# Optimization experiments

Measured on AMD Instinct MI355X. Metric: run time of the kernel, lower is better.

## Reference

```python
import jax, jax.numpy as jnp
import numpy as np

DIM = 1024
FF = 4096
BATCH = 4
SEQ = 2048
EPS = 1e-5


def setup_inputs() -> dict:
    key = jax.random.key(0)
    ks = jax.random.split(key, 8)
    x = jax.random.normal(ks[0], (BATCH, SEQ, DIM), dtype=jnp.float32)
    # phazor init: exp(2j*pi*arange(dim)/dim) * |randn(dim)|
    ang = 2.0 * np.pi * jnp.arange(DIM, dtype=jnp.float32) / DIM
    mag = jnp.abs(jax.random.normal(ks[1], (DIM,), dtype=jnp.float32))
    phazor_re = mag * jnp.cos(ang)
    phazor_im = mag * jnp.sin(ang)
    last_re = jax.random.normal(ks[2], (DIM,), dtype=jnp.float32)
    last_im = jax.random.normal(ks[3], (DIM,), dtype=jnp.float32)
    w1 = jax.random.normal(ks[4], (FF, DIM), dtype=jnp.float32) * DIM ** -0.5
    b1 = jnp.zeros((FF,), dtype=jnp.float32)
    w2 = jax.random.normal(ks[5], (DIM, FF), dtype=jnp.float32) * FF ** -0.5
    b2 = jnp.zeros((DIM,), dtype=jnp.float32)
    return {
        'x': x,
        'ln1_w': jnp.ones((DIM,), jnp.float32), 'ln1_b': jnp.zeros((DIM,), jnp.float32),
        'ln2_w': jnp.ones((DIM,), jnp.float32), 'ln2_b': jnp.zeros((DIM,), jnp.float32),
        'sc_lin': jnp.ones((DIM,), jnp.float32),
        'phazor_re': phazor_re, 'phazor_im': phazor_im,
        'last_re': last_re, 'last_im': last_im,
        'w1': w1, 'b1': b1, 'w2': w2, 'b2': b2,
    }


def _layer_norm(x, w, b):
    mu = jnp.mean(x, axis=-1, keepdims=True)
    var = jnp.mean(jnp.square(x - mu), axis=-1, keepdims=True)
    return (x - mu) * jax.lax.rsqrt(var + EPS) * w + b


def _sconv(x, phazor_re, phazor_im, last_re, last_im):
    B, L, D = x.shape
    dtype = x.dtype
    xc = x.astype(jnp.complex64)
    p_raw = phazor_re + 1j * phazor_im
    # tanh(|p|) * exp(i*angle(p))
    p = (jnp.tanh(jnp.abs(p_raw)) * jnp.exp(1j * jnp.angle(p_raw))).astype(jnp.complex64)
    t = jnp.arange(L)[:, None]
    prog = jnp.power(p[None, :], t)            # [L, D] complex
    filt_fft = jnp.fft.fft(prog, n=2 * L, axis=0)   # [2L, D]
    x_fft = jnp.fft.fft(xc, n=2 * L, axis=1)        # [B, 2L, D]
    conv = jnp.fft.ifft(filt_fft[None] * x_fft, axis=1)[:, :L]  # [B, L, D]
    last = (last_re + 1j * last_im)[None, None, :]  # [1,1,D] broadcast over batch
    conv_with_past = conv + last * prog[None] * p[None, None]
    return conv_with_past.real.astype(dtype)


def reference(x, ln1_w, ln1_b, ln2_w, ln2_b, sc_lin,
              phazor_re, phazor_im, last_re, last_im,
              w1, b1, w2, b2):
    # SConv branch
    x_res = x
    h = _layer_norm(x, ln1_w, ln1_b)
    h = jax.nn.silu(h)
    h = _sconv(h, phazor_re, phazor_im, last_re, last_im)
    h = h * sc_lin
    x = h + x_res
    # FFN branch
    x_res = x
    h = _layer_norm(x, ln2_w, ln2_b)
    h = jax.nn.silu(jnp.einsum('bld,fd->blf', h, w1) + b1)
    h = jnp.einsum('blf,df->bld', h, w2) + b2
    return h + x_res
```

## Files before the change

### kernel.cpp

```cpp
#include <hip/hip_runtime.h>
#include <cmath>


#define DIMD 1024
#define FFD  4096
#define BATCH 4
#define SEQL 2048
#define MROWS (BATCH*SEQL)
#define EPSF 1e-5f
#define CHUNKS 32
#define CLEN (SEQL/CHUNKS)

typedef __attribute__((ext_vector_type(8))) _Float16 half8;
typedef __attribute__((ext_vector_type(4))) _Float16 half4;
typedef __attribute__((ext_vector_type(4))) float    floatx4;

#define H_OFF    0u
#define E_OFF    33554432u
#define SIN_OFF  34603008u
#define H2_OFF   35651584u
#define W1H_OFF  52428800u
#define W2H_OFF  60817408u
#define Y1_OFF   69206016u

__device__ __forceinline__ void load_lds16(const _Float16* g, _Float16* l) {
    __builtin_amdgcn_global_load_lds(
        (const __attribute__((address_space(1))) unsigned int*)g,
        (__attribute__((address_space(3))) unsigned int*)l,
        16, 0, 0);
}

__global__ __launch_bounds__(256)
void cast_f32_f16(const float* __restrict__ src, _Float16* __restrict__ dst) {
    int i = (blockIdx.x * 256 + threadIdx.x) * 4;
    float4 v = *(const float4*)(src + i);
    half4 o;
    o.x = (_Float16)v.x; o.y = (_Float16)v.y; o.z = (_Float16)v.z; o.w = (_Float16)v.w;
    *(half4*)(dst + i) = o;
}

__global__ __launch_bounds__(256)
void ln_kernel(const float* __restrict__ x, const float* __restrict__ w,
               const float* __restrict__ b, float* __restrict__ of,
               _Float16* __restrict__ oh, int mode) {
    const size_t row = blockIdx.x;
    const int tid = threadIdx.x;
    float4 v = *(const float4*)(x + row * DIMD + tid * 4);
    float s = (v.x + v.y) + (v.z + v.w);
    float q = (v.x * v.x + v.y * v.y) + (v.z * v.z + v.w * v.w);
    #pragma unroll
    for (int off = 32; off; off >>= 1) {
        s += __shfl_down(s, off, 64);
        q += __shfl_down(q, off, 64);
    }
    __shared__ float red[8];
    if (!(tid & 63)) { red[tid >> 6] = s; red[4 + (tid >> 6)] = q; }
    __syncthreads();
    s = (red[0] + red[1]) + (red[2] + red[3]);
    q = (red[4] + red[5]) + (red[6] + red[7]);
    const float mu = s * (1.f / DIMD);
    const float rs = rsqrtf(q * (1.f / DIMD) - mu * mu + EPSF);
    float4 wv = *(const float4*)(w + tid * 4);
    float4 bv = *(const float4*)(b + tid * 4);
    float o0 = (v.x - mu) * rs * wv.x + bv.x;
    float o1 = (v.y - mu) * rs * wv.y + bv.y;
    float o2 = (v.z - mu) * rs * wv.z + bv.z;
    float o3 = (v.w - mu) * rs * wv.w + bv.w;
    if (mode == 1) {
        o0 = o0 / (1.f + __expf(-o0));
        o1 = o1 / (1.f + __expf(-o1));
        o2 = o2 / (1.f + __expf(-o2));
        o3 = o3 / (1.f + __expf(-o3));
        float4 ov = {o0, o1, o2, o3};
        *(float4*)(of + row * DIMD + tid * 4) = ov;
    } else {
        half4 hv;
        hv.x = (_Float16)o0; hv.y = (_Float16)o1;
        hv.z = (_Float16)o2; hv.w = (_Float16)o3;
        *(half4*)(oh + row * DIMD + tid * 4) = hv;
    }
}

__device__ __forceinline__ void get_p(const float* pre, const float* pim, int d,
                                      float& pr, float& pi) {
    float re = pre[d], im = pim[d];
    float r = sqrtf(re * re + im * im);
    float t = tanhf(r) / fmaxf(r, 1e-30f);
    pr = re * t; pi = im * t;
}

__global__ __launch_bounds__(256)
void scan_partial(const float* __restrict__ h, const float* __restrict__ pre,
                  const float* __restrict__ pim, float2* __restrict__ e) {
    const int d = blockIdx.x * 256 + threadIdx.x;
    const int c = blockIdx.y;
    const int bb = blockIdx.z;
    float pr, pi; get_p(pre, pim, d, pr, pi);
    float sr = 0.f, si = 0.f;
    const float* hp = h + ((size_t)bb * SEQL + (size_t)c * CLEN) * DIMD + d;
    #pragma unroll 4
    for (int j = 0; j < CLEN; ++j) {
        float hv = hp[(size_t)j * DIMD];
        float nr = pr * sr - pi * si + hv;
        float ni = pr * si + pi * sr;
        sr = nr; si = ni;
    }
    e[((size_t)bb * CHUNKS + c) * DIMD + d] = make_float2(sr, si);
}

__global__ __launch_bounds__(256)
void scan_combine(const float2* __restrict__ e, const float* __restrict__ pre,
                  const float* __restrict__ pim, const float* __restrict__ lre,
                  const float* __restrict__ lim, float2* __restrict__ sv) {
    const int d = blockIdx.x * 256 + threadIdx.x;
    const int bb = blockIdx.y;
    float pr, pi; get_p(pre, pim, d, pr, pi);
    float qr = pr, qi = pi;
    #pragma unroll
    for (int s = 0; s < 6; ++s) {
        float nr = qr * qr - qi * qi;
        float ni = 2.f * qr * qi;
        qr = nr; qi = ni;
    }
    float sr = lre[d], si = lim[d];
    for (int c = 0; c < CHUNKS; ++c) {
        sv[((size_t)bb * CHUNKS + c) * DIMD + d] = make_float2(sr, si);
        float2 ec = e[((size_t)bb * CHUNKS + c) * DIMD + d];
        float nr = qr * sr - qi * si + ec.x;
        float ni = qr * si + qi * sr + ec.y;
        sr = nr; si = ni;
    }
}

__global__ __launch_bounds__(256)
void scan_final(const float* __restrict__ h, const float* __restrict__ x,
                const float* __restrict__ pre, const float* __restrict__ pim,
                const float* __restrict__ sc, const float2* __restrict__ sv,
                float* __restrict__ x2) {
    const int d = blockIdx.x * 256 + threadIdx.x;
    const int c = blockIdx.y;
    const int bb = blockIdx.z;
    float pr, pi; get_p(pre, pim, d, pr, pi);
    float2 s0 = sv[((size_t)bb * CHUNKS + c) * DIMD + d];
    float sr = s0.x, si = s0.y;
    const float scd = sc[d];
    const size_t base = ((size_t)bb * SEQL + (size_t)c * CLEN) * DIMD + d;
    #pragma unroll 4
    for (int j = 0; j < CLEN; ++j) {
        float hv = h[base + (size_t)j * DIMD];
        float nr = pr * sr - pi * si + hv;
        float ni = pr * si + pi * sr;
        sr = nr; si = ni;
        x2[base + (size_t)j * DIMD] = x[base + (size_t)j * DIMD] + scd * sr;
    }
}

#define BM 128
#define BN 128
#define BK 64

__global__ __launch_bounds__(256)
void gemm_bt(const _Float16* __restrict__ A, const _Float16* __restrict__ W,
             const float* __restrict__ bias, _Float16* __restrict__ out_h,
             const float* resid, float* out_f, int N, int K, int epi) {
    __shared__ _Float16 As[BM * BK];
    __shared__ _Float16 Bs[BN * BK];
    const int tid  = threadIdx.x;
    const int lane = tid & 63;
    const int wave = tid >> 6;
    const int wm = (wave >> 1) * 64;
    const int wn = (wave & 1) * 64;
    const size_t m0 = (size_t)blockIdx.y * BM;
    const size_t n0 = (size_t)blockIdx.x * BN;
    const int fr = lane & 15;
    const int quad = lane >> 4;

    const int srow = wave * 32 + (lane >> 3);
    const int ccp  = ((lane & 7) ^ (lane >> 3)) * 8;
    const _Float16* ag = A + (m0 + srow) * (size_t)K + ccp;
    const _Float16* wg = W + (n0 + srow) * (size_t)K + ccp;
    _Float16* asl = &As[(wave * 32) * BK];
    _Float16* bsl = &Bs[(wave * 32) * BK];

    floatx4 acc[4][4] = {};

    for (int k0 = 0; k0 < K; k0 += BK) {
        #pragma unroll
        for (int t = 0; t < 4; ++t) {
            load_lds16(ag + k0 + (size_t)(t * 8) * K, asl + t * 8 * BK);
            load_lds16(wg + k0 + (size_t)(t * 8) * K, bsl + t * 8 * BK);
        }
        __syncthreads();
        #pragma unroll
        for (int kk = 0; kk < BK; kk += 32) {
            half8 af[4], bf[4];
            #pragma unroll
            for (int i = 0; i < 4; ++i) {
                const int slot = (((kk >> 3) + quad) ^ (fr & 7)) * 8;
                af[i] = *(const half8*)(&As[(wm + i * 16 + fr) * BK + slot]);
                bf[i] = *(const half8*)(&Bs[(wn + i * 16 + fr) * BK + slot]);
            }
            #pragma unroll
            for (int i = 0; i < 4; ++i)
                #pragma unroll
                for (int j = 0; j < 4; ++j)
                    acc[i][j] = __builtin_amdgcn_mfma_f32_16x16x32_f16(
                        af[i], bf[j], acc[i][j], 0, 0, 0);
        }
        __syncthreads();
    }

    #pragma unroll
    for (int i = 0; i < 4; ++i) {
        #pragma unroll
        for (int j = 0; j < 4; ++j) {
            #pragma unroll
            for (int r = 0; r < 4; ++r) {
                const size_t gm = m0 + wm + i * 16 + quad * 4 + r;
                const size_t gn = n0 + wn + j * 16 + fr;
                float v = acc[i][j][r] + bias[gn];
                if (epi == 1) {
                    float sl = v / (1.f + __expf(-v));
                    out_h[gm * N + gn] = (_Float16)sl;
                } else {
                    out_f[gm * N + gn] = v + resid[gm * N + gn];
                }
            }
        }
    }
}

extern "C" void kernel_launch(void* const* d_in, const int* in_sizes, int n_in,
                              void* d_out, int out_size, void* d_ws, size_t ws_size,
                              hipStream_t stream) {
    const float* x    = (const float*)d_in[0];
    const float* ln1w = (const float*)d_in[1];
    const float* ln1b = (const float*)d_in[2];
    const float* ln2w = (const float*)d_in[3];
    const float* ln2b = (const float*)d_in[4];
    const float* sc   = (const float*)d_in[5];
    const float* pre  = (const float*)d_in[6];
    const float* pim  = (const float*)d_in[7];
    const float* lre  = (const float*)d_in[8];
    const float* lim  = (const float*)d_in[9];
    const float* w1   = (const float*)d_in[10];
    const float* b1   = (const float*)d_in[11];
    const float* w2   = (const float*)d_in[12];
    const float* b2   = (const float*)d_in[13];

    char* ws = (char*)d_ws;
    float*      h   = (float*)(ws + H_OFF);
    float2*     e   = (float2*)(ws + E_OFF);
    float2*     sv  = (float2*)(ws + SIN_OFF);
    _Float16*   h2  = (_Float16*)(ws + H2_OFF);
    _Float16*   w1h = (_Float16*)(ws + W1H_OFF);
    _Float16*   w2h = (_Float16*)(ws + W2H_OFF);
    _Float16*   y1  = (_Float16*)(ws + Y1_OFF);
    float*      x2  = (float*)d_out;
    float*      outp = (float*)d_out;

    cast_f32_f16<<<dim3(FFD * DIMD / 1024), 256, 0, stream>>>(w1, w1h);
    cast_f32_f16<<<dim3(FFD * DIMD / 1024), 256, 0, stream>>>(w2, w2h);
    ln_kernel<<<dim3(MROWS), 256, 0, stream>>>(x, ln1w, ln1b, h, nullptr, 1);
    scan_partial<<<dim3(DIMD / 256, CHUNKS, BATCH), 256, 0, stream>>>(h, pre, pim, e);
    scan_combine<<<dim3(DIMD / 256, BATCH), 256, 0, stream>>>(e, pre, pim, lre, lim, sv);
    scan_final<<<dim3(DIMD / 256, CHUNKS, BATCH), 256, 0, stream>>>(h, x, pre, pim, sc, sv, x2);
    ln_kernel<<<dim3(MROWS), 256, 0, stream>>>(x2, ln2w, ln2b, nullptr, h2, 2);
    gemm_bt<<<dim3(FFD / BN, MROWS / BM), 256, 0, stream>>>(
        h2, w1h, b1, y1, nullptr, nullptr, FFD, DIMD, 1);
    gemm_bt<<<dim3(DIMD / BN, MROWS / BM), 256, 0, stream>>>(
        y1, w2h, b2, nullptr, x2, outp, DIMD, FFD, 2);
}
```

Baseline: 385.0 us.

## Fuse LN1+SiLU into scan kernels, use 32x32 MFMA and swizzled GEMM grid

```diff
diff --git a/kernel.cpp b/kernel.cpp
--- a/kernel.cpp
+++ b/kernel.cpp
@@ -11,11 +11,12 @@
 #define CHUNKS 32
 #define CLEN (SEQL/CHUNKS)
 
-typedef __attribute__((ext_vector_type(8))) _Float16 half8;
-typedef __attribute__((ext_vector_type(4))) _Float16 half4;
-typedef __attribute__((ext_vector_type(4))) float    floatx4;
-
-#define H_OFF    0u
+typedef __attribute__((ext_vector_type(8)))  _Float16 half8;
+typedef __attribute__((ext_vector_type(4)))  _Float16 half4;
+typedef __attribute__((ext_vector_type(4)))  float    floatx4;
+typedef __attribute__((ext_vector_type(16))) float    floatx16;
+
+#define ST_OFF   0u
 #define E_OFF    33554432u
 #define SIN_OFF  34603008u
 #define H2_OFF   35651584u
@@ -40,9 +41,7 @@
 }
 
 __global__ __launch_bounds__(256)
-void ln_kernel(const float* __restrict__ x, const float* __restrict__ w,
-               const float* __restrict__ b, float* __restrict__ of,
-               _Float16* __restrict__ oh, int mode) {
+void ln_stats(const float* __restrict__ x, float2* __restrict__ st) {
     const size_t row = blockIdx.x;
     const int tid = threadIdx.x;
     float4 v = *(const float4*)(x + row * DIMD + tid * 4);
@@ -56,29 +55,43 @@
     __shared__ float red[8];
     if (!(tid & 63)) { red[tid >> 6] = s; red[4 + (tid >> 6)] = q; }
     __syncthreads();
+    if (tid == 0) {
+        s = (red[0] + red[1]) + (red[2] + red[3]);
+        q = (red[4] + red[5]) + (red[6] + red[7]);
+        const float mu = s * (1.f / DIMD);
+        const float rs = rsqrtf(q * (1.f / DIMD) - mu * mu + EPSF);
+        st[row] = make_float2(mu, rs);
+    }
+}
+
+__global__ __launch_bounds__(256)
+void ln_kernel(const float* __restrict__ x, const float* __restrict__ w,
+               const float* __restrict__ b, _Float16* __restrict__ oh) {
+    const size_t row = blockIdx.x;
+    const int tid = threadIdx.x;
+    float4 v = *(const float4*)(x + row * DIMD + tid * 4);
+    float s = (v.x + v.y) + (v.z + v.w);
+    float q = (v.x * v.x + v.y * v.y) + (v.z * v.z + v.w * v.w);
+    #pragma unroll
+    for (int off = 32; off; off >>= 1) {
+        s += __shfl_down(s, off, 64);
+        q += __shfl_down(q, off, 64);
+    }
+    __shared__ float red[8];
+    if (!(tid & 63)) { red[tid >> 6] = s; red[4 + (tid >> 6)] = q; }
+    __syncthreads();
     s = (red[0] + red[1]) + (red[2] + red[3]);
     q = (red[4] + red[5]) + (red[6] + red[7]);
     const float mu = s * (1.f / DIMD);
     const float rs = rsqrtf(q * (1.f / DIMD) - mu * mu + EPSF);
     float4 wv = *(const float4*)(w + tid * 4);
     float4 bv = *(const float4*)(b + tid * 4);
-    float o0 = (v.x - mu) * rs * wv.x + bv.x;
-    float o1 = (v.y - mu) * rs * wv.y + bv.y;
-    float o2 = (v.z - mu) * rs * wv.z + bv.z;
-    float o3 = (v.w - mu) * rs * wv.w + bv.w;
-    if (mode == 1) {
-        o0 = o0 / (1.f + __expf(-o0));
-        o1 = o1 / (1.f + __expf(-o1));
-        o2 = o2 / (1.f + __expf(-o2));
-        o3 = o3 / (1.f + __expf(-o3));
-        float4 ov = {o0, o1, o2, o3};
-        *(float4*)(of + row * DIMD + tid * 4) = ov;
-    } else {
-        half4 hv;
-        hv.x = (_Float16)o0; hv.y = (_Float16)o1;
-        hv.z = (_Float16)o2; hv.w = (_Float16)o3;
-        *(half4*)(oh + row * DIMD + tid * 4) = hv;
-    }
+    half4 hv;
+    hv.x = (_Float16)((v.x - mu) * rs * wv.x + bv.x);
+    hv.y = (_Float16)((v.y - mu) * rs * wv.y + bv.y);
+    hv.z = (_Float16)((v.z - mu) * rs * wv.z + bv.z);
+    hv.w = (_Float16)((v.w - mu) * rs * wv.w + bv.w);
+    *(half4*)(oh + row * DIMD + tid * 4) = hv;
 }
 
 __device__ __forceinline__ void get_p(const float* pre, const float* pim, int d,
@@ -89,18 +102,28 @@
     pr = re * t; pi = im * t;
 }
 
-__global__ __launch_bounds__(256)
-void scan_partial(const float* __restrict__ h, const float* __restrict__ pre,
-                  const float* __restrict__ pim, float2* __restrict__ e) {
+__device__ __forceinline__ float ln_silu(float xv, float2 st, float wd, float bd) {
+    float o = (xv - st.x) * st.y * wd + bd;
+    return o / (1.f + __expf(-o));
+}
+
+__global__ __launch_bounds__(256)
+void scan_partial(const float* __restrict__ x, const float2* __restrict__ st,
+                  const float* __restrict__ lw, const float* __restrict__ lb,
+                  const float* __restrict__ pre, const float* __restrict__ pim,
+                  float2* __restrict__ e) {
     const int d = blockIdx.x * 256 + threadIdx.x;
     const int c = blockIdx.y;
     const int bb = blockIdx.z;
     float pr, pi; get_p(pre, pim, d, pr, pi);
+    const float wd = lw[d], bd = lb[d];
     float sr = 0.f, si = 0.f;
-    const float* hp = h + ((size_t)bb * SEQL + (size_t)c * CLEN) * DIMD + d;
+    const size_t row0 = (size_t)bb * SEQL + (size_t)c * CLEN;
     #pragma unroll 4
     for (int j = 0; j < CLEN; ++j) {
-        float hv = hp[(size_t)j * DIMD];
+        float xv = x[(row0 + j) * DIMD + d];
+        float2 sj = st[row0 + j];
+        float hv = ln_silu(xv, sj, wd, bd);
         float nr = pr * sr - pi * si + hv;
         float ni = pr * si + pi * sr;
         sr = nr; si = ni;
@@ -133,7 +156,8 @@
 }
 
 __global__ __launch_bounds__(256)
-void scan_final(const float* __restrict__ h, const float* __restrict__ x,
+void scan_final(const float* __restrict__ x, const float2* __restrict__ st,
+                const float* __restrict__ lw, const float* __restrict__ lb,
                 const float* __restrict__ pre, const float* __restrict__ pim,
                 const float* __restrict__ sc, const float2* __restrict__ sv,
                 float* __restrict__ x2) {
@@ -141,89 +165,93 @@
     const int c = blockIdx.y;
     const int bb = blockIdx.z;
     float pr, pi; get_p(pre, pim, d, pr, pi);
+    const float wd = lw[d], bd = lb[d];
     float2 s0 = sv[((size_t)bb * CHUNKS + c) * DIMD + d];
     float sr = s0.x, si = s0.y;
     const float scd = sc[d];
-    const size_t base = ((size_t)bb * SEQL + (size_t)c * CLEN) * DIMD + d;
+    const size_t row0 = (size_t)bb * SEQL + (size_t)c * CLEN;
     #pragma unroll 4
     for (int j = 0; j < CLEN; ++j) {
-        float hv = h[base + (size_t)j * DIMD];
+        float xv = x[(row0 + j) * DIMD + d];
+        float2 sj = st[row0 + j];
+        float hv = ln_silu(xv, sj, wd, bd);
         float nr = pr * sr - pi * si + hv;
         float ni = pr * si + pi * sr;
         sr = nr; si = ni;
-        x2[base + (size_t)j * DIMD] = x[base + (size_t)j * DIMD] + scd * sr;
-    }
-}
-
-#define BM 128
-#define BN 128
-#define BK 64
-
-__global__ __launch_bounds__(256)
-void gemm_bt(const _Float16* __restrict__ A, const _Float16* __restrict__ W,
-             const float* __restrict__ bias, _Float16* __restrict__ out_h,
-             const float* resid, float* out_f, int N, int K, int epi) {
-    __shared__ _Float16 As[BM * BK];
-    __shared__ _Float16 Bs[BN * BK];
+        x2[(row0 + j) * DIMD + d] = xv + scd * sr;
+    }
+}
+
+#define GBM 128
+#define GBN 128
+#define GBK 64
+
+template<int NCOLS, int EPI>
+__global__ __launch_bounds__(256)
+void gemm_128(const _Float16* __restrict__ A, const _Float16* __restrict__ W,
+              const float* __restrict__ bias, _Float16* __restrict__ out_h,
+              const float* __restrict__ resid, float* __restrict__ out_f,
+              int N, int K) {
+    __shared__ _Float16 As[GBM * GBK];
+    __shared__ _Float16 Bs[GBN * GBK];
     const int tid  = threadIdx.x;
     const int lane = tid & 63;
     const int wave = tid >> 6;
     const int wm = (wave >> 1) * 64;
     const int wn = (wave & 1) * 64;
-    const size_t m0 = (size_t)blockIdx.y * BM;
-    const size_t n0 = (size_t)blockIdx.x * BN;
-    const int fr = lane & 15;
-    const int quad = lane >> 4;
+    const int n  = blockIdx.y * gridDim.x + blockIdx.x;
+    const int xc = n & 7, ii = n >> 3;
+    const size_t m0 = (size_t)(xc + ((ii / NCOLS) << 3)) * GBM;
+    const size_t n0 = (size_t)(ii % NCOLS) * GBN;
+    const int r32 = lane & 31;
+    const int kg  = lane >> 5;
 
     const int srow = wave * 32 + (lane >> 3);
     const int ccp  = ((lane & 7) ^ (lane >> 3)) * 8;
     const _Float16* ag = A + (m0 + srow) * (size_t)K + ccp;
     const _Float16* wg = W + (n0 + srow) * (size_t)K + ccp;
-    _Float16* asl = &As[(wave * 32) * BK];
-    _Float16* bsl = &Bs[(wave * 32) * BK];
-
-    floatx4 acc[4][4] = {};
-
-    for (int k0 = 0; k0 < K; k0 += BK) {
+    _Float16* asl = &As[(wave * 32) * GBK];
+    _Float16* bsl = &Bs[(wave * 32) * GBK];
+
+    floatx16 acc[2][2] = {};
+
+    for (int k0 = 0; k0 < K; k0 += GBK) {
         #pragma unroll
         for (int t = 0; t < 4; ++t) {
-            load_lds16(ag + k0 + (size_t)(t * 8) * K, asl + t * 8 * BK);
-            load_lds16(wg + k0 + (size_t)(t * 8) * K, bsl + t * 8 * BK);
+            load_lds16(ag + k0 + (size_t)(t * 8) * K, asl + t * 8 * GBK);
+            load_lds16(wg + k0 + (size_t)(t * 8) * K, bsl + t * 8 * GBK);
         }
         __syncthreads();
         #pragma unroll
-        for (int kk = 0; kk < BK; kk += 32) {
-            half8 af[4], bf[4];
-            #pragma unroll
-            for (int i = 0; i < 4; ++i) {
-                const int slot = (((kk >> 3) + quad) ^ (fr & 7)) * 8;
-                af[i] = *(const half8*)(&As[(wm + i * 16 + fr) * BK + slot]);
-                bf[i] = *(const half8*)(&Bs[(wn + i * 16 + fr) * BK + slot]);
-            }
-            #pragma unroll
-            for (int i = 0; i < 4; ++i)
-                #pragma unroll
-                for (int j = 0; j < 4; ++j)
-                    acc[i][j] = __builtin_amdgcn_mfma_f32_16x16x32_f16(
-                        af[i], bf[j], acc[i][j], 0, 0, 0);
+        for (int ks = 0; ks < 4; ++ks) {
+            const int slot = (((ks << 1) | kg) ^ (r32 & 7)) * 8;
+            half8 af0 = *(const half8*)(&As[(wm +      r32) * GBK + slot]);
+            half8 af1 = *(const half8*)(&As[(wm + 32 + r32) * GBK + slot]);
+            half8 bf0 = *(const half8*)(&Bs[(wn +      r32) * GBK + slot]);
+            half8 bf1 = *(const half8*)(&Bs[(wn + 32 + r32) * GBK + slot]);
+            acc[0][0] = __builtin_amdgcn_mfma_f32_32x32x16_f16(af0, bf0, acc[0][0], 0, 0, 0);
+            acc[0][1] = __builtin_amdgcn_mfma_f32_32x32x16_f16(af0, bf1, acc[0][1], 0, 0, 0);
+            acc[1][0] = __builtin_amdgcn_mfma_f32_32x32x16_f16(af1, bf0, acc[1][0], 0, 0, 0);
+            acc[1][1] = __builtin_amdgcn_mfma_f32_32x32x16_f16(af1, bf1, acc[1][1], 0, 0, 0);
         }
         __syncthreads();
     }
 
     #pragma unroll
-    for (int i = 0; i < 4; ++i) {
+    for (int ib = 0; ib < 2; ++ib) {
         #pragma unroll
-        for (int j = 0; j < 4; ++j) {
+        for (int jb = 0; jb < 2; ++jb) {
+            const size_t gn = n0 + wn + jb * 32 + r32;
+            const float bb = bias[gn];
             #pragma unroll
-            for (int r = 0; r < 4; ++r) {
-                const size_t gm = m0 + wm + i * 16 + quad * 4 + r;
-                const size_t gn = n0 + wn + j * 16 + fr;
-                float v = acc[i][j][r] + bias[gn];
-                if (epi == 1) {
+            for (int r = 0; r < 16; ++r) {
+                const size_t gm = m0 + wm + ib * 32 + (r & 3) + 8 * (r >> 2) + 4 * kg;
+                float v = acc[ib][jb][r] + bb;
+                if (EPI == 1) {
                     float sl = v / (1.f + __expf(-v));
-                    out_h[gm * N + gn] = (_Float16)sl;
+                    out_h[gm * (size_t)N + gn] = (_Float16)sl;
                 } else {
-                    out_f[gm * N + gn] = v + resid[gm * N + gn];
+                    out_f[gm * (size_t)N + gn] = v + resid[gm * (size_t)N + gn];
                 }
             }
         }
@@ -249,7 +277,7 @@
     const float* b2   = (const float*)d_in[13];
 
     char* ws = (char*)d_ws;
-    float*      h   = (float*)(ws + H_OFF);
+    float2*     st  = (float2*)(ws + ST_OFF);
     float2*     e   = (float2*)(ws + E_OFF);
     float2*     sv  = (float2*)(ws + SIN_OFF);
     _Float16*   h2  = (_Float16*)(ws + H2_OFF);
@@ -261,13 +289,16 @@
 
     cast_f32_f16<<<dim3(FFD * DIMD / 1024), 256, 0, stream>>>(w1, w1h);
     cast_f32_f16<<<dim3(FFD * DIMD / 1024), 256, 0, stream>>>(w2, w2h);
-    ln_kernel<<<dim3(MROWS), 256, 0, stream>>>(x, ln1w, ln1b, h, nullptr, 1);
-    scan_partial<<<dim3(DIMD / 256, CHUNKS, BATCH), 256, 0, stream>>>(h, pre, pim, e);
-    scan_combine<<<dim3(DIMD / 256, BATCH), 256, 0, stream>>>(e, pre, pim, lre, lim, sv);
-    scan_final<<<dim3(DIMD / 256, CHUNKS, BATCH), 256, 0, stream>>>(h, x, pre, pim, sc, sv, x2);
-    ln_kernel<<<dim3(MROWS), 256, 0, stream>>>(x2, ln2w, ln2b, nullptr, h2, 2);
-    gemm_bt<<<dim3(FFD / BN, MROWS / BM), 256, 0, stream>>>(
-        h2, w1h, b1, y1, nullptr, nullptr, FFD, DIMD, 1);
-    gemm_bt<<<dim3(DIMD / BN, MROWS / BM), 256, 0, stream>>>(
-        y1, w2h, b2, nullptr, x2, outp, DIMD, FFD, 2);
-}
+    ln_stats<<<dim3(MROWS), 256, 0, stream>>>(x, st);
+    scan_partial<<<dim3(DIMD / 256, CHUNKS, BATCH), 256, 0, stream>>>(
+        x, st, ln1w, ln1b, pre, pim, e);
+    scan_combine<<<dim3(DIMD / 256, BATCH), 256, 0, stream>>>(
+        e, pre, pim, lre, lim, sv);
+    scan_final<<<dim3(DIMD / 256, CHUNKS, BATCH), 256, 0, stream>>>(
+        x, st, ln1w, ln1b, pre, pim, sc, sv, x2);
+    ln_kernel<<<dim3(MROWS), 256, 0, stream>>>(x2, ln2w, ln2b, h2);
+    gemm_128<32, 1><<<dim3(FFD / GBN, MROWS / GBM), 256, 0, stream>>>(
+        h2, w1h, b1, y1, nullptr, nullptr, FFD, DIMD);
+    gemm_128<8, 2><<<dim3(DIMD / GBN, MROWS / GBM), 256, 0, stream>>>(
+        y1, w2h, b2, nullptr, x2, outp, DIMD, FFD);
+}
```

New measurement: 355.5 us. 7.7% less time.
